# Kernel optimization log

Measured on AMD Instinct MI355X. Metric: run time of the kernel, lower is better.

The kernel has to match this reference:

```python
import jax, jax.numpy as jnp
import numpy as np

B, LQ, LK, D = 8, 2048, 2048, 128

def setup_inputs() -> dict:
    key = jax.random.key(0)
    k1, k2, k3, k4 = jax.random.split(key, 4)
    return {
        "query": jax.random.normal(k1, (B, LQ, D), dtype=jnp.float32),
        "key": jax.random.normal(k2, (B, LK, D), dtype=jnp.float32),
        "value": jax.random.normal(k3, (B, LK, D), dtype=jnp.float32),
        "scale_factor": jax.random.normal(k4, (B, LQ, LK), dtype=jnp.float32),
    }

def reference(query, key, value, scale_factor):
    # qk: [B, LQ, LK]
    qk = jnp.einsum("bqd,bkd->bqk", query, key)
    probs = jax.nn.softmax(qk * scale_factor, axis=-1)
    # dropout_p = 0.0 -> identity
    return jnp.einsum("bqk,bkd->bqd", probs, value)
```

## Files before the change

kernel.cpp:

```cpp
#include <hip/hip_runtime.h>


typedef float          f32x4  __attribute__((ext_vector_type(4)));
typedef float          f32x16 __attribute__((ext_vector_type(16)));
typedef _Float16       h16x8  __attribute__((ext_vector_type(8)));
typedef unsigned int   u32x4  __attribute__((ext_vector_type(4)));
typedef unsigned short u16x8  __attribute__((ext_vector_type(8)));

#define LOG2E 1.4426950408889634f

__device__ __forceinline__ float fast_exp2(float x) {
#if __has_builtin(__builtin_amdgcn_exp2f)
    return __builtin_amdgcn_exp2f(x);
#else
    return exp2f(x);
#endif
}

__global__ __launch_bounds__(256)
void prep_all(const float* __restrict__ q, const float* __restrict__ k,
              const float* __restrict__ v,
              unsigned short* __restrict__ qhF, unsigned short* __restrict__ qlF,
              unsigned short* __restrict__ khF, unsigned short* __restrict__ vF) {
    const int bid = blockIdx.x;
    if (bid < 2048) {
        const bool isQ = bid < 1024;
        const int t    = (isQ ? bid : bid - 1024) * 256 + threadIdx.x;
        const int lane = t & 63;
        const int fr   = t >> 6;
        const int s    = fr & 7;
        const int tile = (fr >> 3) & 63;
        const int b    = fr >> 9;
        const int row  = b * 2048 + tile * 32 + (lane & 31);
        const int col  = s * 16 + (lane >> 5) * 8;
        const float* src = (isQ ? q : k) + row * 128 + col;
        float f[8];
        *(f32x4*)&f[0] = *(const f32x4*)src;
        *(f32x4*)&f[4] = *(const f32x4*)(src + 4);
        u16x8 hi, lo;
#pragma unroll
        for (int j = 0; j < 8; ++j) {
            _Float16 h = (_Float16)f[j];
            hi[j] = __builtin_bit_cast(unsigned short, h);
            _Float16 l = (_Float16)(f[j] - (float)h);
            lo[j] = __builtin_bit_cast(unsigned short, l);
        }
        if (isQ) {
            *(u16x8*)(qhF + (size_t)t * 8) = hi;
            *(u16x8*)(qlF + (size_t)t * 8) = lo;
        } else {
            *(u16x8*)(khF + (size_t)t * 8) = hi;
        }
    } else {
        __shared__ unsigned short tile[32 * 132];
        const int id = bid - 2048;
        const int b  = id >> 6;
        const int kc = id & 63;
        const int tid = threadIdx.x;
#pragma unroll
        for (int it = 0; it < 4; ++it) {
            int idx = it * 256 + tid;
            int kk  = idx >> 5;
            int c4  = idx & 31;
            f32x4 val = *(const f32x4*)(v + ((b * 2048 + kc * 32 + kk) * 128 + c4 * 4));
#pragma unroll
            for (int j = 0; j < 4; ++j)
                tile[kk * 132 + c4 * 4 + j] =
                    __builtin_bit_cast(unsigned short, (_Float16)val[j]);
        }
        __syncthreads();
#pragma unroll
        for (int e = 0; e < 2; ++e) {
            int fi   = e * 256 + tid;
            int lane = fi & 63;
            int fr2  = fi >> 6;
            int td   = fr2 >> 1;
            int s2   = fr2 & 1;
            u16x8 o;
#pragma unroll
            for (int j = 0; j < 8; ++j)
                o[j] = tile[(s2 * 16 + (lane >> 5) * 8 + j) * 132 + td * 32 + (lane & 31)];
            *(u16x8*)(vF + ((size_t)((b * 64 + kc) * 8 + fr2) * 64 + lane) * 8) = o;
        }
    }
}

__global__ __launch_bounds__(64)
void flash_fwd(const unsigned short* __restrict__ qhF,
               const unsigned short* __restrict__ qlF,
               const unsigned short* __restrict__ khF,
               const unsigned short* __restrict__ vF,
               const float* __restrict__ scale_g,
               float* __restrict__ out) {
    __shared__ float scbuf[2][32 * 36];

    const int lane = threadIdx.x;
    const int q31  = lane & 31;
    const int h    = lane >> 5;

    const int bid = blockIdx.x;
    const int b   = bid & 7;
    const int qt  = bid >> 3;

    h16x8 qh[8], ql[8];
    {
        const u32x4* qp = (const u32x4*)qhF + ((size_t)(b * 64 + qt) * 8) * 64 + lane;
        const u32x4* lp = (const u32x4*)qlF + ((size_t)(b * 64 + qt) * 8) * 64 + lane;
#pragma unroll
        for (int s = 0; s < 8; ++s) {
            qh[s] = __builtin_bit_cast(h16x8, qp[s * 64]);
            ql[s] = __builtin_bit_cast(h16x8, lp[s * 64]);
        }
    }

    const u32x4* khp = (const u32x4*)khF + ((size_t)(b * 64) * 8) * 64 + lane;
    const u32x4* vp  = (const u32x4*)vF  + ((size_t)(b * 64) * 8) * 64 + lane;

    int scrow[4];
#pragma unroll
    for (int j = 0; j < 4; ++j)
        scrow[j] = (b * 2048 + qt * 32 + j * 8 + (lane >> 3)) * 2048 + (lane & 7) * 4;

    f32x16 oacc[4];
#pragma unroll
    for (int t = 0; t < 4; ++t)
#pragma unroll
        for (int r = 0; r < 16; ++r) oacc[t][r] = 0.f;
    float m_run = -INFINITY, l_run = 0.f;

    h16x8 khr[2][8], vr[2][8];
    f32x4 scv[2][4];

#pragma unroll
    for (int s = 0; s < 8; ++s) khr[0][s] = __builtin_bit_cast(h16x8, khp[s * 64]);
#pragma unroll
    for (int f = 0; f < 8; ++f) vr[0][f]  = __builtin_bit_cast(h16x8, vp[f * 64]);
#pragma unroll
    for (int j = 0; j < 4; ++j) scv[0][j] = *(const f32x4*)(scale_g + scrow[j]);
#pragma unroll
    for (int j = 0; j < 4; ++j) scv[1][j] = *(const f32x4*)(scale_g + scrow[j] + 32);
#pragma unroll
    for (int j = 0; j < 4; ++j)
        *(f32x4*)&scbuf[0][(j * 8 + (lane >> 3)) * 36 + (lane & 7) * 4] = scv[0][j];

    for (int kc2 = 0; kc2 < 32; ++kc2) {
#pragma unroll
        for (int u = 0; u < 2; ++u) {
            const int kc  = kc2 * 2 + u;
            const int cur = u, nxt = u ^ 1;
            const int kn  = (kc + 1) & 63;
            const int ks2 = (kc + 2) & 63;

#pragma unroll
            for (int s = 0; s < 8; ++s)
                khr[nxt][s] = __builtin_bit_cast(h16x8, khp[(kn * 8 + s) * 64]);
#pragma unroll
            for (int f = 0; f < 8; ++f)
                vr[nxt][f]  = __builtin_bit_cast(h16x8, vp[(kn * 8 + f) * 64]);

#pragma unroll
            for (int j = 0; j < 4; ++j)
                *(f32x4*)&scbuf[nxt][(j * 8 + (lane >> 3)) * 36 + (lane & 7) * 4] = scv[nxt][j];

#pragma unroll
            for (int j = 0; j < 4; ++j)
                scv[cur][j] = *(const f32x4*)(scale_g + scrow[j] + ks2 * 32);

            f32x16 S;
#pragma unroll
            for (int r = 0; r < 16; ++r) S[r] = 0.f;
#pragma unroll
            for (int s = 0; s < 8; ++s) {
                S = __builtin_amdgcn_mfma_f32_32x32x16_f16(khr[cur][s], qh[s], S, 0, 0, 0);
                S = __builtin_amdgcn_mfma_f32_32x32x16_f16(khr[cur][s], ql[s], S, 0, 0, 0);
            }

            f32x4 scf[4];
#pragma unroll
            for (int G = 0; G < 4; ++G)
                scf[G] = *(const f32x4*)&scbuf[cur][q31 * 36 + (2 * G + h) * 4];

            float lt[16];
            float mx = -INFINITY;
#pragma unroll
            for (int r = 0; r < 16; ++r) {
                lt[r] = S[r] * scf[r >> 2][r & 3];
                mx = fmaxf(mx, lt[r]);
            }
            mx = fmaxf(mx, __shfl_xor(mx, 32));
            const float m_new = fmaxf(m_run, mx);
            const float al = fast_exp2((m_run - m_new) * LOG2E);
            m_run = m_new;
            float rs = 0.f;
            float p[16];
#pragma unroll
            for (int r = 0; r < 16; ++r) {
                p[r] = fast_exp2((lt[r] - m_new) * LOG2E);
                rs += p[r];
            }
            rs += __shfl_xor(rs, 32);
            l_run = l_run * al + rs;
#pragma unroll
            for (int t = 0; t < 4; ++t)
#pragma unroll
                for (int r = 0; r < 16; ++r) oacc[t][r] *= al;

            unsigned int pa[4], pb[4];
#pragma unroll
            for (int G = 0; G < 4; ++G) {
                pa[G] = __builtin_bit_cast(unsigned int,
                         __builtin_amdgcn_cvt_pkrtz(p[4 * G + 0], p[4 * G + 1]));
                pb[G] = __builtin_bit_cast(unsigned int,
                         __builtin_amdgcn_cvt_pkrtz(p[4 * G + 2], p[4 * G + 3]));
            }
            h16x8 B[2];
#pragma unroll
            for (int s2 = 0; s2 < 2; ++s2) {
                const int Gk = 2 * s2 + h;
                unsigned int sa = h ? pa[2 * s2] : pa[2 * s2 + 1];
                unsigned int sb = h ? pb[2 * s2] : pb[2 * s2 + 1];
                unsigned int xa = (unsigned int)__shfl_xor((int)sa, 32);
                unsigned int xb = (unsigned int)__shfl_xor((int)sb, 32);
                u32x4 w;
                w[0] = h ? xa : pa[Gk];
                w[1] = h ? xb : pb[Gk];
                w[2] = h ? pa[Gk] : xa;
                w[3] = h ? pb[Gk] : xb;
                B[s2] = __builtin_bit_cast(h16x8, w);
            }

#pragma unroll
            for (int t = 0; t < 4; ++t)
#pragma unroll
                for (int s2 = 0; s2 < 2; ++s2)
                    oacc[t] = __builtin_amdgcn_mfma_f32_32x32x16_f16(
                                vr[cur][t * 2 + s2], B[s2], oacc[t], 0, 0, 0);
        }
    }

    const float linv = 1.f / l_run;
    const size_t orow = (size_t)(b * 2048 + qt * 32 + q31) * 128;
#pragma unroll
    for (int t = 0; t < 4; ++t)
#pragma unroll
        for (int G = 0; G < 4; ++G) {
            f32x4 o4;
#pragma unroll
            for (int j = 0; j < 4; ++j) o4[j] = oacc[t][4 * G + j] * linv;
            *(f32x4*)(out + orow + t * 32 + G * 8 + 4 * h) = o4;
        }
}

extern "C" void kernel_launch(void* const* d_in, const int* in_sizes, int n_in,
                              void* d_out, int out_size, void* d_ws, size_t ws_size,
                              hipStream_t stream) {
    const float* q  = (const float*)d_in[0];
    const float* k  = (const float*)d_in[1];
    const float* v  = (const float*)d_in[2];
    const float* sc = (const float*)d_in[3];
    float* out = (float*)d_out;

    char* ws = (char*)d_ws;
    const size_t MB = 1024 * 1024;
    unsigned short* qhF = (unsigned short*)(ws);
    unsigned short* qlF = (unsigned short*)(ws + 4 * MB);
    unsigned short* khF = (unsigned short*)(ws + 8 * MB);
    unsigned short* vF  = (unsigned short*)(ws + 12 * MB);

    prep_all<<<2560, 256, 0, stream>>>(q, k, v, qhF, qlF, khF, vF);
    flash_fwd<<<512, 64, 0, stream>>>(qhF, qlF, khF, vF, sc, out);
}
```

Before: 296.7 us.

## Split key dimension across four waves per block with LDS merge of softmax partials

The flash attention kernel now runs four waves per block. Each wave processes a quarter of the key sequence, and the partial max, sum and output accumulators are combined through shared memory at the end (split-K flash decoding within a block). This raises parallelism from one 64-thread wave per 32-query tile to 256 threads, which should improve latency hiding on 512 blocks. The cost is extra LDS traffic and two barriers for the merge. The hi and lo QK MFMA chains are split into independent accumulators to break the dependency, and prep now stages Q and K through LDS for coalesced loads.

```diff
diff --git a/kernel.cpp b/kernel.cpp
--- a/kernel.cpp
+++ b/kernel.cpp
@@ -5,6 +5,7 @@
 typedef float          f32x16 __attribute__((ext_vector_type(16)));
 typedef _Float16       h16x8  __attribute__((ext_vector_type(8)));
 typedef unsigned int   u32x4  __attribute__((ext_vector_type(4)));
+typedef unsigned short u16x4  __attribute__((ext_vector_type(4)));
 typedef unsigned short u16x8  __attribute__((ext_vector_type(8)));
 
 #define LOG2E 1.4426950408889634f
@@ -17,58 +18,59 @@
 #endif
 }
 
+#define TS 136
 __global__ __launch_bounds__(256)
 void prep_all(const float* __restrict__ q, const float* __restrict__ k,
               const float* __restrict__ v,
               unsigned short* __restrict__ qhF, unsigned short* __restrict__ qlF,
               unsigned short* __restrict__ khF, unsigned short* __restrict__ vF) {
-    const int bid = blockIdx.x;
-    if (bid < 2048) {
-        const bool isQ = bid < 1024;
-        const int t    = (isQ ? bid : bid - 1024) * 256 + threadIdx.x;
-        const int lane = t & 63;
-        const int fr   = t >> 6;
-        const int s    = fr & 7;
-        const int tile = (fr >> 3) & 63;
-        const int b    = fr >> 9;
-        const int row  = b * 2048 + tile * 32 + (lane & 31);
-        const int col  = s * 16 + (lane >> 5) * 8;
-        const float* src = (isQ ? q : k) + row * 128 + col;
-        float f[8];
-        *(f32x4*)&f[0] = *(const f32x4*)src;
-        *(f32x4*)&f[4] = *(const f32x4*)(src + 4);
-        u16x8 hi, lo;
-#pragma unroll
-        for (int j = 0; j < 8; ++j) {
-            _Float16 h = (_Float16)f[j];
-            hi[j] = __builtin_bit_cast(unsigned short, h);
-            _Float16 l = (_Float16)(f[j] - (float)h);
-            lo[j] = __builtin_bit_cast(unsigned short, l);
-        }
-        if (isQ) {
-            *(u16x8*)(qhF + (size_t)t * 8) = hi;
-            *(u16x8*)(qlF + (size_t)t * 8) = lo;
-        } else {
-            *(u16x8*)(khF + (size_t)t * 8) = hi;
+    __shared__ unsigned short hiT[32 * TS];
+    __shared__ unsigned short loT[32 * TS];
+    const int bid  = blockIdx.x;
+    const int kind = bid >> 9;
+    const int id   = bid & 511;
+    const int b    = id >> 6;
+    const int tile = id & 63;
+    const int tid  = threadIdx.x;
+    const float* src = kind == 0 ? q : (kind == 1 ? k : v);
+
+#pragma unroll
+    for (int it = 0; it < 4; ++it) {
+        int idx = it * 256 + tid;
+        int row = idx >> 5;
+        int c4  = idx & 31;
+        f32x4 val = *(const f32x4*)(src + ((size_t)(b * 2048 + tile * 32 + row) * 128 + c4 * 4));
+        u16x4 hi4, lo4;
+#pragma unroll
+        for (int j = 0; j < 4; ++j) {
+            _Float16 hh = (_Float16)val[j];
+            hi4[j] = __builtin_bit_cast(unsigned short, hh);
+            _Float16 ll = (_Float16)(val[j] - (float)hh);
+            lo4[j] = __builtin_bit_cast(unsigned short, ll);
+        }
+        *(u16x4*)&hiT[row * TS + c4 * 4] = hi4;
+        if (kind == 0) *(u16x4*)&loT[row * TS + c4 * 4] = lo4;
+    }
+    __syncthreads();
+
+    if (kind < 2) {
+#pragma unroll
+        for (int e = 0; e < 2; ++e) {
+            int fi   = e * 256 + tid;
+            int lane = fi & 63;
+            int s    = fi >> 6;
+            int off  = (lane & 31) * TS + s * 16 + (lane >> 5) * 8;
+            u16x8 hi8 = *(const u16x8*)&hiT[off];
+            size_t o = ((size_t)(id * 8 + s) * 64 + lane) * 8;
+            if (kind == 0) {
+                u16x8 lo8 = *(const u16x8*)&loT[off];
+                *(u16x8*)(qhF + o) = hi8;
+                *(u16x8*)(qlF + o) = lo8;
+            } else {
+                *(u16x8*)(khF + o) = hi8;
+            }
         }
     } else {
-        __shared__ unsigned short tile[32 * 132];
-        const int id = bid - 2048;
-        const int b  = id >> 6;
-        const int kc = id & 63;
-        const int tid = threadIdx.x;
-#pragma unroll
-        for (int it = 0; it < 4; ++it) {
-            int idx = it * 256 + tid;
-            int kk  = idx >> 5;
-            int c4  = idx & 31;
-            f32x4 val = *(const f32x4*)(v + ((b * 2048 + kc * 32 + kk) * 128 + c4 * 4));
-#pragma unroll
-            for (int j = 0; j < 4; ++j)
-                tile[kk * 132 + c4 * 4 + j] =
-                    __builtin_bit_cast(unsigned short, (_Float16)val[j]);
-        }
-        __syncthreads();
 #pragma unroll
         for (int e = 0; e < 2; ++e) {
             int fi   = e * 256 + tid;
@@ -76,31 +78,42 @@
             int fr2  = fi >> 6;
             int td   = fr2 >> 1;
             int s2   = fr2 & 1;
-            u16x8 o;
+            u16x8 o8;
 #pragma unroll
             for (int j = 0; j < 8; ++j)
-                o[j] = tile[(s2 * 16 + (lane >> 5) * 8 + j) * 132 + td * 32 + (lane & 31)];
-            *(u16x8*)(vF + ((size_t)((b * 64 + kc) * 8 + fr2) * 64 + lane) * 8) = o;
+                o8[j] = hiT[(s2 * 16 + (lane >> 5) * 8 + j) * TS + td * 32 + (lane & 31)];
+            *(u16x8*)(vF + ((size_t)(id * 8 + fr2) * 64 + lane) * 8) = o8;
         }
     }
 }
 
-__global__ __launch_bounds__(64)
+#define LDSZ  68608
+#define MOFF  67584
+#define LOFF  68096
+
+__global__ __launch_bounds__(256, 2)
 void flash_fwd(const unsigned short* __restrict__ qhF,
                const unsigned short* __restrict__ qlF,
                const unsigned short* __restrict__ khF,
                const unsigned short* __restrict__ vF,
                const float* __restrict__ scale_g,
                float* __restrict__ out) {
-    __shared__ float scbuf[2][32 * 36];
-
-    const int lane = threadIdx.x;
+    __shared__ unsigned char smem[LDSZ];
+
+    const int tid  = threadIdx.x;
+    const int wave = tid >> 6;
+    const int lane = tid & 63;
     const int q31  = lane & 31;
     const int h    = lane >> 5;
 
     const int bid = blockIdx.x;
     const int b   = bid & 7;
     const int qt  = bid >> 3;
+
+    float* scb   = (float*)(smem + wave * 9216);
+    float* oex   = (float*)smem;
+    float* mstat = (float*)(smem + MOFF);
+    float* lstat = (float*)(smem + LOFF);
 
     h16x8 qh[8], ql[8];
     {
@@ -113,13 +126,15 @@
         }
     }
 
-    const u32x4* khp = (const u32x4*)khF + ((size_t)(b * 64) * 8) * 64 + lane;
-    const u32x4* vp  = (const u32x4*)vF  + ((size_t)(b * 64) * 8) * 64 + lane;
-
+    const int ck0 = b * 64 + wave * 16;
+    const u32x4* khp = (const u32x4*)khF + ((size_t)ck0 * 8) * 64 + lane;
+    const u32x4* vp  = (const u32x4*)vF  + ((size_t)ck0 * 8) * 64 + lane;
+
+    const int kbase = wave * 512;
     int scrow[4];
 #pragma unroll
     for (int j = 0; j < 4; ++j)
-        scrow[j] = (b * 2048 + qt * 32 + j * 8 + (lane >> 3)) * 2048 + (lane & 7) * 4;
+        scrow[j] = (b * 2048 + qt * 32 + j * 8 + (lane >> 3)) * 2048 + kbase + (lane & 7) * 4;
 
     f32x16 oacc[4];
 #pragma unroll
@@ -141,15 +156,15 @@
     for (int j = 0; j < 4; ++j) scv[1][j] = *(const f32x4*)(scale_g + scrow[j] + 32);
 #pragma unroll
     for (int j = 0; j < 4; ++j)
-        *(f32x4*)&scbuf[0][(j * 8 + (lane >> 3)) * 36 + (lane & 7) * 4] = scv[0][j];
-
-    for (int kc2 = 0; kc2 < 32; ++kc2) {
+        *(f32x4*)&scb[(j * 8 + (lane >> 3)) * 36 + (lane & 7) * 4] = scv[0][j];
+
+    for (int kc2 = 0; kc2 < 8; ++kc2) {
 #pragma unroll
         for (int u = 0; u < 2; ++u) {
             const int kc  = kc2 * 2 + u;
             const int cur = u, nxt = u ^ 1;
-            const int kn  = (kc + 1) & 63;
-            const int ks2 = (kc + 2) & 63;
+            const int kn  = (kc + 1) & 15;
+            const int ks2 = (kc + 2) & 15;
 
 #pragma unroll
             for (int s = 0; s < 8; ++s)
@@ -160,25 +175,26 @@
 
 #pragma unroll
             for (int j = 0; j < 4; ++j)
-                *(f32x4*)&scbuf[nxt][(j * 8 + (lane >> 3)) * 36 + (lane & 7) * 4] = scv[nxt][j];
+                *(f32x4*)&scb[nxt * 1152 + (j * 8 + (lane >> 3)) * 36 + (lane & 7) * 4] = scv[nxt][j];
 
 #pragma unroll
             for (int j = 0; j < 4; ++j)
                 scv[cur][j] = *(const f32x4*)(scale_g + scrow[j] + ks2 * 32);
 
-            f32x16 S;
-#pragma unroll
-            for (int r = 0; r < 16; ++r) S[r] = 0.f;
+            f32x16 Sa, Sb;
+#pragma unroll
+            for (int r = 0; r < 16; ++r) { Sa[r] = 0.f; Sb[r] = 0.f; }
 #pragma unroll
             for (int s = 0; s < 8; ++s) {
-                S = __builtin_amdgcn_mfma_f32_32x32x16_f16(khr[cur][s], qh[s], S, 0, 0, 0);
-                S = __builtin_amdgcn_mfma_f32_32x32x16_f16(khr[cur][s], ql[s], S, 0, 0, 0);
-            }
+                Sa = __builtin_amdgcn_mfma_f32_32x32x16_f16(khr[cur][s], qh[s], Sa, 0, 0, 0);
+                Sb = __builtin_amdgcn_mfma_f32_32x32x16_f16(khr[cur][s], ql[s], Sb, 0, 0, 0);
+            }
+            f32x16 S = Sa + Sb;
 
             f32x4 scf[4];
 #pragma unroll
             for (int G = 0; G < 4; ++G)
-                scf[G] = *(const f32x4*)&scbuf[cur][q31 * 36 + (2 * G + h) * 4];
+                scf[G] = *(const f32x4*)&scb[cur * 1152 + q31 * 36 + (2 * G + h) * 4];
 
             float lt[16];
             float mx = -INFINITY;
@@ -213,7 +229,7 @@
                 pb[G] = __builtin_bit_cast(unsigned int,
                          __builtin_amdgcn_cvt_pkrtz(p[4 * G + 2], p[4 * G + 3]));
             }
-            h16x8 B[2];
+            h16x8 Bf[2];
 #pragma unroll
             for (int s2 = 0; s2 < 2; ++s2) {
                 const int Gk = 2 * s2 + h;
@@ -226,7 +242,7 @@
                 w[1] = h ? xb : pb[Gk];
                 w[2] = h ? pa[Gk] : xa;
                 w[3] = h ? pb[Gk] : xb;
-                B[s2] = __builtin_bit_cast(h16x8, w);
+                Bf[s2] = __builtin_bit_cast(h16x8, w);
             }
 
 #pragma unroll
@@ -234,21 +250,50 @@
 #pragma unroll
                 for (int s2 = 0; s2 < 2; ++s2)
                     oacc[t] = __builtin_amdgcn_mfma_f32_32x32x16_f16(
-                                vr[cur][t * 2 + s2], B[s2], oacc[t], 0, 0, 0);
-        }
-    }
-
-    const float linv = 1.f / l_run;
-    const size_t orow = (size_t)(b * 2048 + qt * 32 + q31) * 128;
-#pragma unroll
-    for (int t = 0; t < 4; ++t)
-#pragma unroll
-        for (int G = 0; G < 4; ++G) {
-            f32x4 o4;
-#pragma unroll
-            for (int j = 0; j < 4; ++j) o4[j] = oacc[t][4 * G + j] * linv;
-            *(f32x4*)(out + orow + t * 32 + G * 8 + 4 * h) = o4;
-        }
+                                vr[cur][t * 2 + s2], Bf[s2], oacc[t], 0, 0, 0);
+        }
+    }
+
+    if (h == 0) mstat[wave * 32 + q31] = m_run;
+    __syncthreads();
+    {
+        float M = mstat[q31];
+#pragma unroll
+        for (int w = 1; w < 4; ++w) M = fmaxf(M, mstat[w * 32 + q31]);
+        const float al = fast_exp2((m_run - M) * LOG2E);
+        if (h == 0) lstat[wave * 32 + q31] = l_run * al;
+#pragma unroll
+        for (int t = 0; t < 4; ++t)
+#pragma unroll
+            for (int G = 0; G < 4; ++G) {
+                f32x4 v4;
+#pragma unroll
+                for (int j = 0; j < 4; ++j) v4[j] = oacc[t][4 * G + j] * al;
+                *(f32x4*)&oex[wave * 4224 + q31 * 132 + t * 32 + G * 8 + 4 * h] = v4;
+            }
+    }
+    __syncthreads();
+    {
+        const int qq   = tid >> 3;
+        const int dblk = tid & 7;
+        const float linv = 1.f / (lstat[qq] + lstat[32 + qq] + lstat[64 + qq] + lstat[96 + qq]);
+#pragma unroll
+        for (int jj = 0; jj < 2; ++jj) {
+            const int d = dblk * 16 + jj * 8;
+#pragma unroll
+            for (int half = 0; half < 2; ++half) {
+                const int dd = d + half * 4;
+                f32x4 acc = *(const f32x4*)&oex[qq * 132 + dd];
+#pragma unroll
+                for (int w = 1; w < 4; ++w) {
+                    f32x4 pv = *(const f32x4*)&oex[w * 4224 + qq * 132 + dd];
+                    acc[0] += pv[0]; acc[1] += pv[1]; acc[2] += pv[2]; acc[3] += pv[3];
+                }
+                acc[0] *= linv; acc[1] *= linv; acc[2] *= linv; acc[3] *= linv;
+                *(f32x4*)(out + (size_t)(b * 2048 + qt * 32 + qq) * 128 + dd) = acc;
+            }
+        }
+    }
 }
 
 extern "C" void kernel_launch(void* const* d_in, const int* in_sizes, int n_in,
@@ -267,6 +312,6 @@
     unsigned short* khF = (unsigned short*)(ws + 8 * MB);
     unsigned short* vF  = (unsigned short*)(ws + 12 * MB);
 
-    prep_all<<<2560, 256, 0, stream>>>(q, k, v, qhF, qlF, khF, vF);
-    flash_fwd<<<512, 64, 0, stream>>>(qhF, qlF, khF, vF, sc, out);
+    prep_all<<<1536, 256, 0, stream>>>(q, k, v, qhF, qlF, khF, vF);
+    flash_fwd<<<512, 256, 0, stream>>>(qhF, qlF, khF, vF, sc, out);
 }
```

After: 361.2 us. 1.22x slower.
